# Performance work log

Hardware: AMD Instinct MI355X
Metric: run time of the kernel (lower is better)

## Reference

```python
import jax, jax.numpy as jnp
import numpy as np

NHEADS = 64; EMB = 2048; STATE = 128; KCONV = 4; NGROUPS = 1
HEAD_DIM = 64; CHUNK = 128; EPS = 1e-6
INTER = NHEADS * HEAD_DIM                  # int(expand*emb_dim) = 4096
CONV_DIM = INTER + 2 * NGROUPS * STATE     # 4352
PROJ = INTER + CONV_DIM + NHEADS           # 8512
BATCH = 2; SEQ = 2048


def segsum(x):
    # x: (..., T) -> (..., T, T) stable segment sums; -inf strictly above diagonal
    T = x.shape[-1]
    xe = jnp.broadcast_to(x[..., None], x.shape + (T,))
    m_strict = jnp.tril(jnp.ones((T, T), bool), -1)
    s = jnp.cumsum(jnp.where(m_strict, xe, 0.0), axis=-2)
    m_incl = jnp.tril(jnp.ones((T, T), bool), 0)
    return jnp.where(m_incl, s, -jnp.inf)


def setup_inputs() -> dict:
    key = jax.random.key(0)
    ks = jax.random.split(key, 6)
    x = jax.random.normal(ks[0], (BATCH, SEQ, EMB), jnp.float32)
    in_proj_w = jax.random.normal(ks[1], (PROJ, EMB), jnp.float32) * 0.02
    conv_w = jax.random.normal(ks[2], (CONV_DIM, 1, KCONV), jnp.float32) * 0.2
    conv_b = jax.random.normal(ks[3], (CONV_DIM,), jnp.float32) * 0.1
    dt_bias = jnp.ones((NHEADS,), jnp.float32)
    A_log = jnp.log(jnp.arange(1, NHEADS + 1, dtype=jnp.float32))
    D = jnp.ones((NHEADS,), jnp.float32)
    norm_w = jnp.ones((INTER,), jnp.float32)
    out_proj_w = jax.random.normal(ks[4], (EMB, INTER), jnp.float32) * 0.02
    mask = jnp.ones((BATCH, 1, SEQ), jnp.int32)  # shape[1]==1 -> masking is a no-op, as in torch path
    return {"x": x, "in_proj_w": in_proj_w, "conv_w": conv_w, "conv_b": conv_b,
            "dt_bias": dt_bias, "A_log": A_log, "D": D, "norm_w": norm_w,
            "out_proj_w": out_proj_w, "mask": mask}


def reference(x, in_proj_w, conv_w, conv_b, dt_bias, A_log, D, norm_w, out_proj_w, mask):
    b, s, _ = x.shape
    proj = x @ in_proj_w.T                                    # (b,s,PROJ)
    gate = proj[..., :INTER]
    hBC = proj[..., INTER:INTER + CONV_DIM]
    dt = proj[..., INTER + CONV_DIM:]                         # (b,s,H)

    # causal depthwise conv1d (torch pads k-1 both sides then truncates to seq_len == left-pad k-1)
    conv = jax.lax.conv_general_dilated(
        hBC.transpose(0, 2, 1), conv_w, (1,), [(KCONV - 1, 0)],
        feature_group_count=CONV_DIM)
    hBC = jax.nn.silu((conv + conv_b[None, :, None]).transpose(0, 2, 1))

    hid = hBC[..., :INTER]
    Bm = hBC[..., INTER:INTER + NGROUPS * STATE]
    Cm = hBC[..., INTER + NGROUPS * STATE:]

    A = -jnp.exp(A_log)                                       # (H,)
    dt = jax.nn.softplus(dt + dt_bias)                        # clamp(0,inf) is a no-op after softplus

    hid = hid.reshape(b, s, NHEADS, HEAD_DIM)
    pad = (CHUNK - s % CHUNK) % CHUNK
    D_res = D[:, None] * jnp.pad(hid, ((0, 0), (0, pad), (0, 0), (0, 0)))
    hid = hid * dt[..., None]
    A_s = A * dt                                              # (b,s,H)
    Bm = jnp.tile(Bm.reshape(b, s, NGROUPS, STATE), (1, 1, NHEADS // NGROUPS, 1))
    Cm = jnp.tile(Cm.reshape(b, s, NGROUPS, STATE), (1, 1, NHEADS // NGROUPS, 1))

    def chunkify(t):
        t = jnp.pad(t, ((0, 0), (0, pad)) + ((0, 0),) * (t.ndim - 2))
        return t.reshape(b, -1, CHUNK, *t.shape[2:])

    hid_c, A_c, B_c, C_c = (chunkify(t) for t in (hid, A_s, Bm, Cm))
    A_c = A_c.transpose(0, 3, 1, 2)                           # (b,H,c,l)
    A_cum = jnp.cumsum(A_c, -1)

    # intra-chunk (diagonal blocks)
    L = jnp.exp(segsum(A_c))                                  # (b,H,c,l,l)
    G = jnp.einsum('bclhn,bcshn->bhcls', C_c, B_c)
    Y_diag = jnp.einsum('bhcls,bcshp->bclhp', G * L, hid_c)

    # per-chunk end states
    decay_states = jnp.exp(A_cum[..., -1:] - A_cum)           # (b,H,c,l)
    states = jnp.einsum('bclhn,bhcl,bclhp->bchpn', B_c, decay_states, hid_c)

    # inter-chunk recurrence
    A_last = jnp.pad(A_cum[..., -1], ((0, 0), (0, 0), (1, 0)))  # (b,H,c+1)
    decay_chunk = jnp.exp(segsum(A_last))                     # (b,H,c+1,c+1)
    states = jnp.concatenate([jnp.zeros_like(states[:, :1]), states], axis=1)
    new_states = jnp.einsum('bhzc,bchpn->bzhpn', decay_chunk, states)
    states = new_states[:, :-1]                               # states entering each chunk

    # off-diagonal (cross-chunk) contribution
    state_decay = jnp.exp(A_cum)                              # (b,H,c,l)
    Y_off = jnp.einsum('bclhn,bchpn,bhcl->bclhp', C_c, states, state_decay)

    y = (Y_diag + Y_off).reshape(b, -1, NHEADS, HEAD_DIM) + D_res
    y = y[:, :s].reshape(b, s, INTER)

    # gated RMSNorm
    yg = y * jax.nn.silu(gate)
    yn = norm_w * (yg * jax.lax.rsqrt(jnp.mean(yg * yg, -1, keepdims=True) + EPS))
    return yn @ out_proj_w.T
```

## Files before the change

kernel.cpp:

```cpp
#include <hip/hip_runtime.h>
#include <math.h>

#define NHEADS   64
#define EMB      2048
#define STATE    128
#define KCONV    4
#define HEAD_DIM 64
#define CHUNK    128
#define SEQL     2048
#define NBATCH   2
#define NCH      (SEQL/CHUNK)
#define INTER    (NHEADS*HEAD_DIM)
#define CONVD    (INTER + 2*STATE)
#define PROJD    (INTER + CONVD + NHEADS)
#define ROWS     (NBATCH*SEQL)
#define EPSV     1e-6f

__device__ __forceinline__ float sigmoidf_(float x){ return 1.f/(1.f+__expf(-x)); }

__device__ __forceinline__ float b2f(ushort u){
  union{float f; unsigned u;} x; x.u = ((unsigned)u)<<16; return x.f;
}
__device__ __forceinline__ ushort f2b(float f){
  union{float f; unsigned u;} x; x.f=f;
  unsigned r = x.u + 0x7FFFu + ((x.u>>16)&1u);
  return (ushort)(r>>16);
}
__device__ __forceinline__ float4 ld4(const float* p){ return *(const float4*)p; }
__device__ __forceinline__ float4 ld4(const ushort* p){
  ushort4 v = *(const ushort4*)p;
  return make_float4(b2f(v.x),b2f(v.y),b2f(v.z),b2f(v.w));
}
__device__ __forceinline__ void st4(float* p, float4 v){ *(float4*)p = v; }
__device__ __forceinline__ void st4(ushort* p, float4 v){
  ushort4 o; o.x=f2b(v.x); o.y=f2b(v.y); o.z=f2b(v.z); o.w=f2b(v.w);
  *(ushort4*)p = o;
}
__device__ __forceinline__ void stc(float* p, float v){ *p = v; }
__device__ __forceinline__ void stc(ushort* p, float v){ *p = f2b(v); }

__global__ __launch_bounds__(256) void f32_to_bf16_kernel(
    const float* __restrict__ in, ushort* __restrict__ out, long n)
{
  long i = ((long)blockIdx.x*256 + threadIdx.x) * 8;
  if (i >= n) return;
  float4 a = *(const float4*)(in + i);
  float4 b = *(const float4*)(in + i + 4);
  st4(out + i, a);
  st4(out + i + 4, b);
}

typedef __attribute__((ext_vector_type(8))) short short8v;
typedef __attribute__((ext_vector_type(4))) float float4v;

#define GLL16(g, l) __builtin_amdgcn_global_load_lds( \
    (const __attribute__((address_space(1))) void*)(g), \
    (__attribute__((address_space(3))) void*)(l), 16, 0, 0)

template<typename TC>
__global__ __launch_bounds__(256) void gemm_mfma_bt(
    const ushort* __restrict__ A, int lda,
    const ushort* __restrict__ B, int ldb,
    TC* __restrict__ C, int ldc,
    int N, int K)
{
  __shared__ ushort As[128*32];
  __shared__ ushort Bs[128*32];
  const int t = threadIdx.x;
  const int lt = t & 63, w = t >> 6;
  const int wr = w >> 1, wc = w & 1;

  const int nwg = gridDim.x * gridDim.y;
  int orig = blockIdx.x + gridDim.x * blockIdx.y;
  int tile = orig;
  if ((nwg & 7) == 0) tile = (orig & 7) * (nwg >> 3) + (orig >> 3);
  const int m0 = (tile / gridDim.x) * 128;
  const int n0 = (tile % gridDim.x) * 128;

  float4v acc[4][4];
  #pragma unroll
  for (int i=0;i<4;++i)
    #pragma unroll
    for (int j=0;j<4;++j) acc[i][j] = float4v{0.f,0.f,0.f,0.f};

  const int srow = t >> 2;
  const int scol = (t & 3) * 8;
  const int bn0 = min(n0 + srow, N-1);
  const int bn1 = min(n0 + 64 + srow, N-1);
  const long aoff0 = (long)(m0 + srow) * lda + scol;
  const long aoff1 = (long)(m0 + 64 + srow) * lda + scol;
  const long boff0 = (long)bn0 * ldb + scol;
  const long boff1 = (long)bn1 * ldb + scol;
  const int lr = lt & 15, lk = (lt >> 4) * 8;

  for (int k0 = 0; k0 < K; k0 += 32) {
    GLL16(A + aoff0 + k0, As + t*8);
    GLL16(A + aoff1 + k0, As + 2048 + t*8);
    GLL16(B + boff0 + k0, Bs + t*8);
    GLL16(B + boff1 + k0, Bs + 2048 + t*8);
    __syncthreads();
    short8v af[4], bf[4];
    #pragma unroll
    for (int i = 0; i < 4; ++i) {
      af[i] = *(const short8v*)(As + (wr*64 + i*16 + lr)*32 + lk);
      bf[i] = *(const short8v*)(Bs + (wc*64 + i*16 + lr)*32 + lk);
    }
    #pragma unroll
    for (int i = 0; i < 4; ++i)
      #pragma unroll
      for (int j = 0; j < 4; ++j)
        acc[i][j] = __builtin_amdgcn_mfma_f32_16x16x32_bf16(af[i], bf[j], acc[i][j], 0, 0, 0);
    __syncthreads();
  }

  const int cr = (lt >> 4) * 4;
  const int cc = lt & 15;
  #pragma unroll
  for (int i = 0; i < 4; ++i) {
    #pragma unroll
    for (int j = 0; j < 4; ++j) {
      int col = n0 + wc*64 + j*16 + cc;
      if (col < N) {
        #pragma unroll
        for (int r = 0; r < 4; ++r) {
          int row = m0 + wr*64 + i*16 + cr + r;
          stc(C + (long)row*ldc + col, acc[i][j][r]);
        }
      }
    }
  }
}

#define BM 128
#define BN 128
#define BKK 16

template<typename TA, typename TB, typename TC>
__global__ __launch_bounds__(256) void gemm_bnt(
    const TA* __restrict__ A, int lda, long sA,
    const TB* __restrict__ B, int ldb, long sB,
    TC* __restrict__ C, int ldc, long sC,
    int M, int N, int K)
{
  A += (long)blockIdx.z * sA;
  B += (long)blockIdx.z * sB;
  C += (long)blockIdx.z * sC;
  const int n0 = blockIdx.x * BN;
  const int m0 = blockIdx.y * BM;
  __shared__ float As[BKK][BM+4];
  __shared__ float Bs[BKK][BN+4];
  const int t = threadIdx.x;
  const int tx = t & 15, ty = t >> 4;
  float acc[8][8];
  #pragma unroll
  for (int i=0;i<8;++i)
    #pragma unroll
    for (int j=0;j<8;++j) acc[i][j]=0.f;

  for (int k0 = 0; k0 < K; k0 += BKK) {
    #pragma unroll
    for (int i = 0; i < 2; ++i) {
      int f = t + i*256;
      int row = f >> 2, kq = (f & 3) << 2;
      float4 v = ld4(A + (long)(m0+row)*lda + (k0 + kq));
      As[kq+0][row]=v.x; As[kq+1][row]=v.y; As[kq+2][row]=v.z; As[kq+3][row]=v.w;
      int gn = n0 + row;
      float4 w = make_float4(0.f,0.f,0.f,0.f);
      if (gn < N) w = ld4(B + (long)gn*ldb + (k0 + kq));
      Bs[kq+0][row]=w.x; Bs[kq+1][row]=w.y; Bs[kq+2][row]=w.z; Bs[kq+3][row]=w.w;
    }
    __syncthreads();
    #pragma unroll
    for (int k = 0; k < BKK; ++k) {
      float a[8], b[8];
      *(float4*)&a[0] = *(const float4*)&As[k][ty*8];
      *(float4*)&a[4] = *(const float4*)&As[k][ty*8+4];
      *(float4*)&b[0] = *(const float4*)&Bs[k][tx*8];
      *(float4*)&b[4] = *(const float4*)&Bs[k][tx*8+4];
      #pragma unroll
      for (int i = 0; i < 8; ++i)
        #pragma unroll
        for (int j = 0; j < 8; ++j)
          acc[i][j] = fmaf(a[i], b[j], acc[i][j]);
    }
    __syncthreads();
  }
  #pragma unroll
  for (int i = 0; i < 8; ++i) {
    int gm = m0 + ty*8 + i;
    #pragma unroll
    for (int j = 0; j < 8; j += 4) {
      int gn = n0 + tx*8 + j;
      if (gn < N)
        st4(C + (long)gm*ldc + gn,
            make_float4(acc[i][j],acc[i][j+1],acc[i][j+2],acc[i][j+3]));
    }
  }
}

__global__ __launch_bounds__(256) void conv_silu_kernel(
    const ushort* __restrict__ proj, const float* __restrict__ cw,
    const float* __restrict__ cb, ushort* __restrict__ out)
{
  const int C4 = CONVD/4;
  long idx = (long)blockIdx.x*256 + threadIdx.x;
  if (idx >= (long)ROWS*C4) return;
  int r = (int)(idx / C4);
  int c = (int)(idx % C4) * 4;
  int tt = r & (SEQL-1);
  float4 bv = *(const float4*)(cb + c);
  float acc0=bv.x, acc1=bv.y, acc2=bv.z, acc3=bv.w;
  float4 w0 = *(const float4*)(cw + (c+0)*KCONV);
  float4 w1 = *(const float4*)(cw + (c+1)*KCONV);
  float4 w2 = *(const float4*)(cw + (c+2)*KCONV);
  float4 w3 = *(const float4*)(cw + (c+3)*KCONV);
  const float wj0[4] = {w0.x,w0.y,w0.z,w0.w};
  const float wj1[4] = {w1.x,w1.y,w1.z,w1.w};
  const float wj2[4] = {w2.x,w2.y,w2.z,w2.w};
  const float wj3[4] = {w3.x,w3.y,w3.z,w3.w};
  #pragma unroll
  for (int j = 0; j < KCONV; ++j) {
    int tr = tt - (KCONV-1) + j;
    if (tr >= 0) {
      float4 v = ld4(proj + (long)(r - (KCONV-1) + j)*PROJD + INTER + c);
      acc0 = fmaf(v.x, wj0[j], acc0);
      acc1 = fmaf(v.y, wj1[j], acc1);
      acc2 = fmaf(v.z, wj2[j], acc2);
      acc3 = fmaf(v.w, wj3[j], acc3);
    }
  }
  float4 o;
  o.x = acc0 * sigmoidf_(acc0);
  o.y = acc1 * sigmoidf_(acc1);
  o.z = acc2 * sigmoidf_(acc2);
  o.w = acc3 * sigmoidf_(acc3);
  st4(out + (long)r*CONVD + c, o);
}

__global__ void dt_kernel(const ushort* __restrict__ proj,
                          const float* __restrict__ dt_bias,
                          float* __restrict__ dtb)
{
  int idx = blockIdx.x*256 + threadIdx.x;
  if (idx >= ROWS*NHEADS) return;
  int r = idx >> 6, h = idx & 63;
  float xv = b2f(proj[(long)r*PROJD + INTER + CONVD + h]) + dt_bias[h];
  dtb[idx] = fmaxf(xv, 0.f) + __logf(1.f + __expf(-fabsf(xv)));
}

__global__ void acum_kernel(const float* __restrict__ dtb,
                            const float* __restrict__ A_log,
                            float* __restrict__ acum)
{
  int idx = blockIdx.x*256 + threadIdx.x;
  if (idx >= NBATCH*NCH*NHEADS) return;
  int h = idx & 63, bc = idx >> 6;
  float Ah = -__expf(A_log[h]);
  const float* d = dtb + (long)bc*CHUNK*NHEADS + h;
  float* o = acum + (long)idx*CHUNK;
  float acc = 0.f;
  for (int l = 0; l < CHUNK; ++l) { acc = fmaf(Ah, d[l*NHEADS], acc); o[l] = acc; }
}

__global__ __launch_bounds__(256) void states_mfma_kernel(
    const ushort* __restrict__ conv, const float* __restrict__ dtb,
    const float* __restrict__ acum, ushort* __restrict__ states)
{
  const int h = blockIdx.x, c = blockIdx.y, b = blockIdx.z;
  const int bc = b*NCH + c;
  const long r0 = (long)bc*CHUNK;
  __shared__ ushort Ahi[64][136];
  __shared__ ushort Alo[64][136];
  __shared__ ushort Bt[128][136];
  __shared__ float arow[CHUNK];
  __shared__ float wrow[CHUNK];
  const int t = threadIdx.x;
  const int lt = t & 63, w = t >> 6;
  const int lr = lt & 15, lk = (lt >> 4) * 8;

  if (t < CHUNK) arow[t] = acum[((long)bc*NHEADS + h)*CHUNK + t];
  __syncthreads();
  if (t < CHUNK) wrow[t] = dtb[(r0 + t)*NHEADS + h] * __expf(arow[CHUNK-1] - arow[t]);
  __syncthreads();

  for (int i = t; i < CHUNK*HEAD_DIM/8; i += 256) {
    int l = i >> 3, p0 = (i & 7) * 8;
    short8v v = *(const short8v*)(conv + (r0+l)*CONVD + h*HEAD_DIM + p0);
    float wl = wrow[l];
    #pragma unroll
    for (int j = 0; j < 8; ++j) {
      float f = b2f((ushort)v[j]) * wl;
      ushort hb = f2b(f);
      Ahi[p0+j][l] = hb;
      Alo[p0+j][l] = f2b(f - b2f(hb));
    }
  }
  for (int i = t; i < CHUNK*STATE/8; i += 256) {
    int l = i >> 4, n0 = (i & 15) * 8;
    short8v v = *(const short8v*)(conv + (r0+l)*CONVD + INTER + n0);
    #pragma unroll
    for (int j = 0; j < 8; ++j) Bt[n0+j][l] = (ushort)v[j];
  }
  __syncthreads();

  float4v acc[8];
  #pragma unroll
  for (int j = 0; j < 8; ++j) acc[j] = float4v{0,0,0,0};
  #pragma unroll
  for (int kk = 0; kk < 4; ++kk) {
    short8v ahi = *(const short8v*)&Ahi[w*16 + lr][kk*32 + lk];
    short8v alo = *(const short8v*)&Alo[w*16 + lr][kk*32 + lk];
    #pragma unroll
    for (int nj = 0; nj < 8; ++nj) {
      short8v bv = *(const short8v*)&Bt[nj*16 + lr][kk*32 + lk];
      acc[nj] = __builtin_amdgcn_mfma_f32_16x16x32_bf16(ahi, bv, acc[nj], 0, 0, 0);
      acc[nj] = __builtin_amdgcn_mfma_f32_16x16x32_bf16(alo, bv, acc[nj], 0, 0, 0);
    }
  }
  ushort* so = states + ((long)bc*NHEADS + h)*HEAD_DIM*STATE;
  const int cr = (lt >> 4) * 4, cc = lt & 15;
  #pragma unroll
  for (int nj = 0; nj < 8; ++nj)
    #pragma unroll
    for (int r = 0; r < 4; ++r)
      so[(w*16 + cr + r)*STATE + nj*16 + cc] = f2b(acc[nj][r]);
}

__global__ __launch_bounds__(256) void scan_kernel(
    ushort* __restrict__ states, const float* __restrict__ acum)
{
  const int bh = blockIdx.x;
  const int b = bh >> 6, h = bh & 63;
  const int t = threadIdx.x;
  float acc[32];
  #pragma unroll
  for (int i=0;i<32;++i) acc[i]=0.f;
  for (int c = 0; c < NCH; ++c) {
    const long bch = ((long)(b*NCH + c)*NHEADS + h);
    float lam = __expf(acum[bch*CHUNK + CHUNK-1]);
    ushort* sb = states + bch*HEAD_DIM*STATE;
    #pragma unroll
    for (int i = 0; i < 32; ++i) {
      float v = b2f(sb[t + i*256]);
      sb[t + i*256] = f2b(acc[i]);
      acc[i] = fmaf(acc[i], lam, v);
    }
  }
}

__global__ __launch_bounds__(256) void y_mfma_kernel(
    const ushort* __restrict__ conv, const float* __restrict__ dtb,
    const float* __restrict__ acum, const float* __restrict__ G,
    const ushort* __restrict__ states, const float* __restrict__ Dp,
    ushort* __restrict__ proj)
{
  const int h = blockIdx.x;
  const int c = blockIdx.y >> 1, mh = blockIdx.y & 1;
  const int b = blockIdx.z;
  const int bc = b*NCH + c;
  const int mbase = mh * 64;
  const long r0 = (long)bc*CHUNK;

  __shared__ float  Af[64][132];
  __shared__ ushort B0[64][136];
  __shared__ ushort B1[64][136];
  __shared__ float arow[CHUNK];
  __shared__ float dtr[CHUNK];
  __shared__ float el[64];

  const int t = threadIdx.x;
  const int lt = t & 63, w = t >> 6;
  const int lr = lt & 15, lk = (lt >> 4) * 8;

  if (t < CHUNK) {
    arow[t] = acum[((long)bc*NHEADS + h)*CHUNK + t];
    dtr[t]  = dtb[(r0 + t)*NHEADS + h];
  }
  __syncthreads();

  if (t < 64) el[t] = __expf(arow[mbase + t]);
  for (int i = t; i < CHUNK*HEAD_DIM/8; i += 256) {
    int s = i >> 3, p0 = (i & 7) * 8;
    short8v v = *(const short8v*)(conv + (r0+s)*CONVD + h*HEAD_DIM + p0);
    #pragma unroll
    for (int j = 0; j < 8; ++j) B0[p0+j][s] = (ushort)v[j];
  }
  {
    const ushort* stb = states + ((long)bc*NHEADS + h)*HEAD_DIM*STATE;
    for (int i = t; i < HEAD_DIM*STATE/8; i += 256) {
      int p = i >> 4, n0 = (i & 15) * 8;
      *(short8v*)&B1[p][n0] = *(const short8v*)(stb + p*STATE + n0);
    }
  }
  {
    const float* Gb = G + (long)bc*CHUNK*CHUNK;
    for (int i = t; i < 64*CHUNK; i += 256) {
      int ll = i >> 7, s = i & 127;
      int l = mbase + ll;
      float wv = 0.f;
      if (s <= l) wv = Gb[l*CHUNK + s] * __expf(arow[l] - arow[s]) * dtr[s];
      Af[ll][s] = wv;
    }
  }
  __syncthreads();

  float4v acc1[4], acc2[4];
  #pragma unroll
  for (int j = 0; j < 4; ++j) { acc1[j] = float4v{0,0,0,0}; acc2[j] = float4v{0,0,0,0}; }

  #pragma unroll
  for (int kk = 0; kk < 4; ++kk) {
    const float* ap = &Af[w*16 + lr][kk*32 + lk];
    float a8[8];
    *(float4*)&a8[0] = *(const float4*)ap;
    *(float4*)&a8[4] = *(const float4*)(ap + 4);
    short8v ahi, alo;
    #pragma unroll
    for (int e = 0; e < 8; ++e) {
      ushort hb = f2b(a8[e]);
      float rem = a8[e] - b2f(hb);
      ahi[e] = (short)hb;
      alo[e] = (short)f2b(rem);
    }
    #pragma unroll
    for (int nj = 0; nj < 4; ++nj) {
      short8v bfv = *(const short8v*)&B0[nj*16 + lr][kk*32 + lk];
      acc1[nj] = __builtin_amdgcn_mfma_f32_16x16x32_bf16(ahi, bfv, acc1[nj], 0, 0, 0);
      acc1[nj] = __builtin_amdgcn_mfma_f32_16x16x32_bf16(alo, bfv, acc1[nj], 0, 0, 0);
    }
  }
  __syncthreads();

  for (int i = t; i < 64*STATE; i += 256) {
    int ll = i >> 7, n = i & 127;
    Af[ll][n] = b2f(conv[(r0 + mbase + ll)*CONVD + INTER + STATE + n]);
  }
  __syncthreads();

  #pragma unroll
  for (int kk = 0; kk < 4; ++kk) {
    const float* ap = &Af[w*16 + lr][kk*32 + lk];
    float a8[8];
    *(float4*)&a8[0] = *(const float4*)ap;
    *(float4*)&a8[4] = *(const float4*)(ap + 4);
    short8v ahi;
    #pragma unroll
    for (int e = 0; e < 8; ++e) ahi[e] = (short)f2b(a8[e]);
    #pragma unroll
    for (int nj = 0; nj < 4; ++nj) {
      short8v bfv = *(const short8v*)&B1[nj*16 + lr][kk*32 + lk];
      acc2[nj] = __builtin_amdgcn_mfma_f32_16x16x32_bf16(ahi, bfv, acc2[nj], 0, 0, 0);
    }
  }

  const float Dh = Dp[h];
  const int cr = (lt >> 4) * 4, cc = lt & 15;
  #pragma unroll
  for (int nj = 0; nj < 4; ++nj) {
    int p = nj*16 + cc;
    #pragma unroll
    for (int r = 0; r < 4; ++r) {
      int ll = w*16 + cr + r;
      float hid_raw = b2f(B0[p][mbase + ll]);
      float yv = acc1[nj][r] + el[ll]*acc2[nj][r] + Dh*hid_raw;
      proj[(r0 + mbase + ll)*PROJD + INTER + h*HEAD_DIM + p] = f2b(yv);
    }
  }
}

__global__ __launch_bounds__(256) void gate_norm_kernel(
    ushort* __restrict__ proj, const float* __restrict__ nw)
{
  const int r = blockIdx.x;
  const int t = threadIdx.x;
  __shared__ float red[256];
  ushort* gate = proj + (long)r*PROJD;
  ushort* y = gate + INTER;
  float vals[16];
  float ss = 0.f;
  #pragma unroll
  for (int k = 0; k < 4; ++k) {
    int j = (t + k*256) * 4;
    float4 g = ld4(gate + j);
    float4 yv = ld4(y + j);
    float v0 = yv.x * g.x * sigmoidf_(g.x);
    float v1 = yv.y * g.y * sigmoidf_(g.y);
    float v2 = yv.z * g.z * sigmoidf_(g.z);
    float v3 = yv.w * g.w * sigmoidf_(g.w);
    vals[k*4+0]=v0; vals[k*4+1]=v1; vals[k*4+2]=v2; vals[k*4+3]=v3;
    ss += v0*v0 + v1*v1 + v2*v2 + v3*v3;
  }
  red[t] = ss;
  __syncthreads();
  for (int sft = 128; sft > 0; sft >>= 1) {
    if (t < sft) red[t] += red[t+sft];
    __syncthreads();
  }
  float scale = rsqrtf(red[0] / (float)INTER + EPSV);
  #pragma unroll
  for (int k = 0; k < 4; ++k) {
    int j = (t + k*256) * 4;
    float4 w = *(const float4*)(nw + j);
    st4(y + j, make_float4(vals[k*4+0]*scale*w.x, vals[k*4+1]*scale*w.y,
                           vals[k*4+2]*scale*w.z, vals[k*4+3]*scale*w.w));
  }
}

extern "C" void kernel_launch(void* const* d_in, const int* in_sizes, int n_in,
                              void* d_out, int out_size, void* d_ws, size_t ws_size,
                              hipStream_t stream) {
  const float* x       = (const float*)d_in[0];
  const float* Wi      = (const float*)d_in[1];
  const float* cw      = (const float*)d_in[2];
  const float* cb      = (const float*)d_in[3];
  const float* dt_bias = (const float*)d_in[4];
  const float* A_log   = (const float*)d_in[5];
  const float* Dp      = (const float*)d_in[6];
  const float* nw      = (const float*)d_in[7];
  const float* Wo      = (const float*)d_in[8];
  float* out = (float*)d_out;

  ushort* projb = (ushort*)d_ws;
  ushort* R     = projb + (size_t)ROWS*PROJD;
  ushort* xb    = R;
  ushort* Wib   = R + (size_t)ROWS*EMB;
  ushort* Wob   = R;
  ushort* convb = R;
  float*  dtb   = (float*)(convb + (size_t)ROWS*CONVD);
  float*  acum  = dtb  + (size_t)ROWS*NHEADS;
  float*  Gb    = acum + (size_t)NBATCH*NCH*NHEADS*CHUNK;
  ushort* st    = (ushort*)(Gb + (size_t)NBATCH*NCH*CHUNK*CHUNK);

  size_t need = (size_t)ROWS*PROJD*2 + (size_t)ROWS*CONVD*2
              + (size_t)ROWS*NHEADS*4 + (size_t)NBATCH*NCH*NHEADS*CHUNK*4
              + (size_t)NBATCH*NCH*CHUNK*CHUNK*4
              + (size_t)NBATCH*NCH*NHEADS*HEAD_DIM*STATE*2;
  if (ws_size < need) return;

  f32_to_bf16_kernel<<<(int)((long)ROWS*EMB/8/256), 256, 0, stream>>>(x, xb, (long)ROWS*EMB);
  f32_to_bf16_kernel<<<(int)((long)PROJD*EMB/8/256), 256, 0, stream>>>(Wi, Wib, (long)PROJD*EMB);
  gemm_mfma_bt<ushort><<<dim3((PROJD+127)/128, ROWS/128), 256, 0, stream>>>(
      xb, EMB, Wib, EMB, projb, PROJD, PROJD, EMB);
  conv_silu_kernel<<<(int)(((long)ROWS*(CONVD/4)+255)/256), 256, 0, stream>>>(
      projb, cw, cb, convb);
  dt_kernel<<<ROWS*NHEADS/256, 256, 0, stream>>>(projb, dt_bias, dtb);
  acum_kernel<<<(NBATCH*NCH*NHEADS+255)/256, 256, 0, stream>>>(dtb, A_log, acum);
  gemm_bnt<ushort,ushort,float><<<dim3(1,1,NBATCH*NCH), 256, 0, stream>>>(
      convb + INTER + STATE, CONVD, (long)CHUNK*CONVD,
      convb + INTER,         CONVD, (long)CHUNK*CONVD,
      Gb, CHUNK, (long)CHUNK*CHUNK, CHUNK, CHUNK, CHUNK);
  states_mfma_kernel<<<dim3(NHEADS, NCH, NBATCH), 256, 0, stream>>>(convb, dtb, acum, st);
  scan_kernel<<<NBATCH*NHEADS, 256, 0, stream>>>(st, acum);
  y_mfma_kernel<<<dim3(NHEADS, NCH*2, NBATCH), 256, 0, stream>>>(
      convb, dtb, acum, Gb, st, Dp, projb);
  gate_norm_kernel<<<ROWS, 256, 0, stream>>>(projb, nw);
  f32_to_bf16_kernel<<<(int)((long)EMB*INTER/8/256), 256, 0, stream>>>(Wo, Wob, (long)EMB*INTER);
  gemm_mfma_bt<float><<<dim3(EMB/128, ROWS/128), 256, 0, stream>>>(
      projb + INTER, PROJD, Wob, INTER, out, EMB, EMB, INTER);
}
```

Measured before the change: 661.8 us.

## Replace MFMA GEMM with 4-stage pipelined, swizzled 128x256 tile kernel

Replaces the single-buffered 128x128 bf16 MFMA GEMM with a 512-thread, 128x256-tile kernel. It uses a 4-deep LDS ring of async global-to-LDS loads with explicit vmcnt waits, and XOR-swizzled LDS addressing to avoid bank conflicts. MFMA issue is split into two halves with s_setprio to overlap LDS reads with matrix math. Both projection GEMMs use it. The larger LDS footprint (96KB) and the removed guard on the tile remap (which now assumes grid size divisible by 8) add occupancy and correctness risks.

Result: slower. 737.0 us (+11.4%).

```diff
diff --git a/kernel.cpp b/kernel.cpp
--- a/kernel.cpp
+++ b/kernel.cpp
@@ -57,25 +57,41 @@
     (const __attribute__((address_space(1))) void*)(g), \
     (__attribute__((address_space(3))) void*)(l), 16, 0, 0)
 
+#define SBAR asm volatile("s_barrier" ::: "memory")
+
 template<typename TC>
-__global__ __launch_bounds__(256) void gemm_mfma_bt(
+__global__ __launch_bounds__(512, 2) void gemm_pipe_bt(
     const ushort* __restrict__ A, int lda,
     const ushort* __restrict__ B, int ldb,
     TC* __restrict__ C, int ldc,
     int N, int K)
 {
-  __shared__ ushort As[128*32];
-  __shared__ ushort Bs[128*32];
+  __shared__ ushort ASb[4][128*32];
+  __shared__ ushort BSb[4][256*32];
   const int t = threadIdx.x;
   const int lt = t & 63, w = t >> 6;
-  const int wr = w >> 1, wc = w & 1;
+  const int wr = w >> 2, wc = w & 3;
 
   const int nwg = gridDim.x * gridDim.y;
   int orig = blockIdx.x + gridDim.x * blockIdx.y;
-  int tile = orig;
-  if ((nwg & 7) == 0) tile = (orig & 7) * (nwg >> 3) + (orig >> 3);
+  int tile = (orig & 7) * (nwg >> 3) + (orig >> 3);
   const int m0 = (tile / gridDim.x) * 128;
-  const int n0 = (tile % gridDim.x) * 128;
+  const int n0 = (tile % gridDim.x) * 256;
+
+  const int rs = t >> 2;
+  const int cs = ((t & 3) ^ ((rs >> 1) & 3)) * 8;
+  const long asrc  = (long)(m0 + rs) * lda + cs;
+  const long bsrc0 = (long)min(n0 + rs, N-1) * ldb + cs;
+  const long bsrc1 = (long)min(n0 + 128 + rs, N-1) * ldb + cs;
+  const int ldst = t * 16;
+
+  auto STAGE = [&](int kt) {
+    int b = kt & 3;
+    long ko = (long)kt * 32;
+    GLL16(A + asrc  + ko, (char*)ASb[b] + ldst);
+    GLL16(B + bsrc0 + ko, (char*)BSb[b] + ldst);
+    GLL16(B + bsrc1 + ko, (char*)BSb[b] + 8192 + ldst);
+  };
 
   float4v acc[4][4];
   #pragma unroll
@@ -83,48 +99,64 @@
     #pragma unroll
     for (int j=0;j<4;++j) acc[i][j] = float4v{0.f,0.f,0.f,0.f};
 
-  const int srow = t >> 2;
-  const int scol = (t & 3) * 8;
-  const int bn0 = min(n0 + srow, N-1);
-  const int bn1 = min(n0 + 64 + srow, N-1);
-  const long aoff0 = (long)(m0 + srow) * lda + scol;
-  const long aoff1 = (long)(m0 + 64 + srow) * lda + scol;
-  const long boff0 = (long)bn0 * ldb + scol;
-  const long boff1 = (long)bn1 * ldb + scol;
-  const int lr = lt & 15, lk = (lt >> 4) * 8;
-
-  for (int k0 = 0; k0 < K; k0 += 32) {
-    GLL16(A + aoff0 + k0, As + t*8);
-    GLL16(A + aoff1 + k0, As + 2048 + t*8);
-    GLL16(B + boff0 + k0, Bs + t*8);
-    GLL16(B + boff1 + k0, Bs + 2048 + t*8);
-    __syncthreads();
-    short8v af[4], bf[4];
-    #pragma unroll
-    for (int i = 0; i < 4; ++i) {
-      af[i] = *(const short8v*)(As + (wr*64 + i*16 + lr)*32 + lk);
-      bf[i] = *(const short8v*)(Bs + (wc*64 + i*16 + lr)*32 + lk);
-    }
-    #pragma unroll
-    for (int i = 0; i < 4; ++i)
+  const int NT = K >> 5;
+  STAGE(0); STAGE(1); STAGE(2);
+
+  const int lr = lt & 15, lks = lt >> 4;
+  for (int kt = 0; kt < NT; ++kt) {
+    if (kt + 3 < NT) STAGE(kt + 3);
+    if (kt < NT-3)       asm volatile("s_waitcnt vmcnt(9)" ::: "memory");
+    else if (kt == NT-3) asm volatile("s_waitcnt vmcnt(6)" ::: "memory");
+    else if (kt == NT-2) asm volatile("s_waitcnt vmcnt(3)" ::: "memory");
+    else                 asm volatile("s_waitcnt vmcnt(0)" ::: "memory");
+    SBAR;
+    const char* ab = (const char*)ASb[kt & 3];
+    const char* bb = (const char*)BSb[kt & 3];
+    short8v afr[4], bfr[4];
+    #pragma unroll
+    for (int mi = 0; mi < 4; ++mi) {
+      int rr = wr*64 + mi*16 + lr;
+      afr[mi] = *(const short8v*)(ab + rr*64 + ((lks ^ ((rr>>1)&3))*16));
+    }
+    #pragma unroll
+    for (int nj = 0; nj < 2; ++nj) {
+      int rr = wc*64 + nj*16 + lr;
+      bfr[nj] = *(const short8v*)(bb + rr*64 + ((lks ^ ((rr>>1)&3))*16));
+    }
+    __builtin_amdgcn_s_setprio(1);
+    #pragma unroll
+    for (int mi = 0; mi < 4; ++mi)
       #pragma unroll
-      for (int j = 0; j < 4; ++j)
-        acc[i][j] = __builtin_amdgcn_mfma_f32_16x16x32_bf16(af[i], bf[j], acc[i][j], 0, 0, 0);
-    __syncthreads();
+      for (int nj = 0; nj < 2; ++nj)
+        acc[mi][nj] = __builtin_amdgcn_mfma_f32_16x16x32_bf16(afr[mi], bfr[nj], acc[mi][nj], 0, 0, 0);
+    __builtin_amdgcn_s_setprio(0);
+    #pragma unroll
+    for (int nj = 2; nj < 4; ++nj) {
+      int rr = wc*64 + nj*16 + lr;
+      bfr[nj] = *(const short8v*)(bb + rr*64 + ((lks ^ ((rr>>1)&3))*16));
+    }
+    __builtin_amdgcn_s_setprio(1);
+    #pragma unroll
+    for (int mi = 0; mi < 4; ++mi)
+      #pragma unroll
+      for (int nj = 2; nj < 4; ++nj)
+        acc[mi][nj] = __builtin_amdgcn_mfma_f32_16x16x32_bf16(afr[mi], bfr[nj], acc[mi][nj], 0, 0, 0);
+    __builtin_amdgcn_s_setprio(0);
+    SBAR;
   }
 
   const int cr = (lt >> 4) * 4;
   const int cc = lt & 15;
   #pragma unroll
-  for (int i = 0; i < 4; ++i) {
-    #pragma unroll
-    for (int j = 0; j < 4; ++j) {
-      int col = n0 + wc*64 + j*16 + cc;
+  for (int mi = 0; mi < 4; ++mi) {
+    #pragma unroll
+    for (int nj = 0; nj < 4; ++nj) {
+      int col = n0 + wc*64 + nj*16 + cc;
       if (col < N) {
         #pragma unroll
         for (int r = 0; r < 4; ++r) {
-          int row = m0 + wr*64 + i*16 + cr + r;
-          stc(C + (long)row*ldc + col, acc[i][j][r]);
+          int row = m0 + wr*64 + mi*16 + cr + r;
+          stc(C + (long)row*ldc + col, acc[mi][nj][r]);
         }
       }
     }
@@ -539,7 +571,7 @@
 
   f32_to_bf16_kernel<<<(int)((long)ROWS*EMB/8/256), 256, 0, stream>>>(x, xb, (long)ROWS*EMB);
   f32_to_bf16_kernel<<<(int)((long)PROJD*EMB/8/256), 256, 0, stream>>>(Wi, Wib, (long)PROJD*EMB);
-  gemm_mfma_bt<ushort><<<dim3((PROJD+127)/128, ROWS/128), 256, 0, stream>>>(
+  gemm_pipe_bt<ushort><<<dim3(34, 32), 512, 0, stream>>>(
       xb, EMB, Wib, EMB, projb, PROJD, PROJD, EMB);
   conv_silu_kernel<<<(int)(((long)ROWS*(CONVD/4)+255)/256), 256, 0, stream>>>(
       projb, cw, cb, convb);
@@ -555,6 +587,6 @@
       convb, dtb, acum, Gb, st, Dp, projb);
   gate_norm_kernel<<<ROWS, 256, 0, stream>>>(projb, nw);
   f32_to_bf16_kernel<<<(int)((long)EMB*INTER/8/256), 256, 0, stream>>>(Wo, Wob, (long)EMB*INTER);
-  gemm_mfma_bt<float><<<dim3(EMB/128, ROWS/128), 256, 0, stream>>>(
+  gemm_pipe_bt<float><<<dim3(8, 32), 512, 0, stream>>>(
       projb + INTER, PROJD, Wob, INTER, out, EMB, EMB, INTER);
 }
```
